# Performance work log

Hardware: AMD Instinct MI355X
Metric: run time of the kernel (lower is better)

The kernel has to match this reference:

```python
import jax, jax.numpy as jnp
import numpy as np

# Static problem dims (match setup_inputs / torch max()+1 derivation)
N = 2_000_000      # atoms
NALT = 8           # alternatives
B, C, R = 8, 4, 512  # batch, chains, residues
N_ATOM_TYPES = 500
VDW_COL = 0        # property_hashings['solvenergy_props']['VdW']
PADDING_INDEX = -1
BACKBONE_ATOMS = (0, 1, 2, 3)


def setup_inputs() -> dict:
    key = jax.random.key(0)
    k1, k2, k3, k4, k5, k6, k7, k8 = jax.random.split(key, 8)
    at_name = jax.random.randint(k1, (N,), 0, 40)      # atom type hashes (first 4 = backbone)
    batch = jax.random.randint(k2, (N,), 0, B)
    chain = jax.random.randint(k3, (N,), 0, C)
    resnum = jax.random.randint(k4, (N,), 0, R)
    atom_description = jnp.stack([at_name, batch, chain, resnum], axis=1).astype(jnp.int64)
    return {
        "coords": jax.random.normal(k5, (N, 3), dtype=jnp.float32),
        "atom_description": atom_description,
        "alternativeMask": jax.random.randint(k6, (N, NALT), 0, 2).astype(bool),
        "facc": jax.random.uniform(k7, (N, NALT), dtype=jnp.float32),
        "atom_Properties": jax.random.uniform(k8, (N_ATOM_TYPES, 8), dtype=jnp.float32),
        "weight": jnp.zeros((1,), dtype=jnp.float32),
    }


def reference(coords, atom_description, alternativeMask, facc, atom_Properties, weight):
    at_name = atom_description[:, 0]
    b_idx = atom_description[:, 1]
    c_idx = atom_description[:, 2]
    r_idx = atom_description[:, 3]

    # is_backbone: OR over backbone atom hashes
    bb = jnp.asarray(BACKBONE_ATOMS)
    is_backbone = (at_name[:, None] == bb[None, :]).any(axis=-1)  # [N]

    # bindToAtoms: gather VdW property, masked multiply by max(facc, 0)
    sa = jnp.maximum(facc, jnp.float32(0.0))                 # [N, NALT]
    vdw = atom_Properties[at_name, VDW_COL]                  # [N]
    atomE = jnp.where(alternativeMask, vdw[:, None] * sa, jnp.float32(0.0))
    atomE = atomE * (1.0 - jnp.tanh(weight[0])) * 0.3        # [N, NALT]

    # bindToResi: masked scatter-add into [B, C, R, NALT]
    valid = r_idx != PADDING_INDEX
    mc_vals = jnp.where((is_backbone & valid)[:, None], atomE, jnp.float32(0.0))
    sc_vals = jnp.where((~is_backbone & valid)[:, None], atomE, jnp.float32(0.0))
    zeros = jnp.zeros((B, C, R, NALT), dtype=jnp.float32)
    finalMC = zeros.at[b_idx, c_idx, r_idx].add(mc_vals)
    finalSC = zeros.at[b_idx, c_idx, r_idx].add(sc_vals)
    return finalMC, finalSC
```

## Files before the change

### kernel.cpp

```cpp
#include <hip/hip_runtime.h>
#include <hip/hip_bf16.h>
#include <math.h>

#define NALT      8
#define BDIM      8
#define CDIM      4
#define RDIM      512
#define OUT_HALF  (BDIM * CDIM * RDIM * NALT)
#define OUT_TOTAL (2 * OUT_HALF)

#define NBUCKET   32
#define BLK_ATOMS 1024
#define AITER     4
#define NWAVE     4
#define LSLOTS    8192


__device__ __forceinline__ unsigned int pack_bf16_2(float a, float b) {
    unsigned int ua = __float_as_uint(a);
    unsigned int ub = __float_as_uint(b);
    ua = (ua + 0x7fffu + ((ua >> 16) & 1u)) >> 16;
    ub = (ub + 0x7fffu + ((ub >> 16) & 1u)) >> 16;
    return ua | (ub << 16);
}

__global__ void __launch_bounds__(256) vdw_count_kernel(
    const int4*   __restrict__ desc,
    unsigned int* __restrict__ PW,
    unsigned short* __restrict__ hdr,
    int n)
{
    __shared__ unsigned int cw[NWAVE][NBUCKET];
    __shared__ unsigned int base[NBUCKET + 1];
    const int tid = threadIdx.x;
    const int w   = tid >> 6;
    if (tid < NWAVE * NBUCKET) cw[tid >> 5][tid & 31] = 0;
    __syncthreads();

    const int a0 = blockIdx.x * BLK_ATOMS;
    #pragma unroll
    for (int it = 0; it < AITER; ++it) {
        const int a = a0 + it * 256 + tid;
        if (a < n) {
            const int4 d = desc[a];
            if (d.w != -1) atomicAdd(&cw[w][d.y * CDIM + d.z], 1);
        }
    }
    __syncthreads();

    if (tid < NBUCKET) {
        unsigned int s = 0;
        unsigned int pref[NWAVE];
        #pragma unroll
        for (int ww = 0; ww < NWAVE; ++ww) { pref[ww] = s; s += cw[ww][tid]; }
        base[tid] = s;
        #pragma unroll
        for (int ww = 0; ww < NWAVE; ++ww) cw[ww][tid] = pref[ww];
    }
    __syncthreads();
    if (tid == 0) {
        unsigned int run = 0;
        #pragma unroll
        for (int j = 0; j < NBUCKET; ++j) { const unsigned int t = base[j]; base[j] = run; run += t; }
        base[NBUCKET] = run;
    }
    __syncthreads();

    if (tid < NBUCKET) {
        #pragma unroll
        for (int ww = 0; ww < NWAVE; ++ww)
            PW[(size_t)blockIdx.x * (NWAVE * NBUCKET) + ww * NBUCKET + tid] =
                base[tid] + cw[ww][tid];
    }
    if (tid <= NBUCKET) hdr[blockIdx.x * 64 + tid] = (unsigned short)base[tid];
}

__global__ void __launch_bounds__(256) vdw_compact_kernel(
    const int4*   __restrict__ desc,
    const int4*   __restrict__ mask,
    const float4* __restrict__ facc,
    const float*  __restrict__ props,
    const float*  __restrict__ weight,
    const unsigned int* __restrict__ PW,
    unsigned short* __restrict__ lidxArr,
    uint4*        __restrict__ valArr,
    int n)
{
    __shared__ unsigned short s_lidx[BLK_ATOMS];
    __shared__ uint4          s_val[BLK_ATOMS];
    __shared__ unsigned int   cw[NWAVE][NBUCKET];

    const int tid  = threadIdx.x;
    const int w    = tid >> 6;
    const int lane = tid & 63;
    if (lane < NBUCKET) cw[w][lane] = 0;

    const float scale = (1.0f - tanhf(weight[0])) * 0.3f;
    const int a0 = blockIdx.x * BLK_ATOMS;
    const unsigned int* myPW = PW + (size_t)blockIdx.x * (NWAVE * NBUCKET) + w * NBUCKET;

    int4   d_[AITER];
    float4 f0_[AITER], f1_[AITER];
    int4   m0_[AITER], m1_[AITER];
    bool   ok[AITER];
    #pragma unroll
    for (int it = 0; it < AITER; ++it) {
        const int a  = a0 + it * 256 + tid;
        ok[it] = (a < n);
        const int aa = ok[it] ? a : (n - 1);
        d_[it]  = desc[aa];
        f0_[it] = facc[aa * 2 + 0];
        f1_[it] = facc[aa * 2 + 1];
        m0_[it] = mask[aa * 2 + 0];
        m1_[it] = mask[aa * 2 + 1];
    }

    #pragma unroll
    for (int it = 0; it < AITER; ++it) {
        const int4 d = d_[it];
        if (!ok[it] || d.w == -1) continue;
        const int bkt  = d.y * CDIM + d.z;
        const float vs = props[d.x * 8] * scale;
        const int lidx = ((d.x < 4) ? 0 : 4096) + d.w * 8;

        const float4 f0 = f0_[it], f1 = f1_[it];
        const int4   m0 = m0_[it], m1 = m1_[it];
        const float v0 = m0.x ? vs * fmaxf(f0.x, 0.0f) : 0.0f;
        const float v1 = m0.y ? vs * fmaxf(f0.y, 0.0f) : 0.0f;
        const float v2 = m0.z ? vs * fmaxf(f0.z, 0.0f) : 0.0f;
        const float v3 = m0.w ? vs * fmaxf(f0.w, 0.0f) : 0.0f;
        const float v4 = m1.x ? vs * fmaxf(f1.x, 0.0f) : 0.0f;
        const float v5 = m1.y ? vs * fmaxf(f1.y, 0.0f) : 0.0f;
        const float v6 = m1.z ? vs * fmaxf(f1.z, 0.0f) : 0.0f;
        const float v7 = m1.w ? vs * fmaxf(f1.w, 0.0f) : 0.0f;

        const unsigned int rank = atomicAdd(&cw[w][bkt], 1u);
        const unsigned int pos  = myPW[bkt] + rank;
        s_lidx[pos] = (unsigned short)lidx;
        s_val[pos]  = make_uint4(pack_bf16_2(v0, v1), pack_bf16_2(v2, v3),
                                 pack_bf16_2(v4, v5), pack_bf16_2(v6, v7));
    }
    __syncthreads();

    unsigned int* ldst = (unsigned int*)(lidxArr + (size_t)blockIdx.x * BLK_ATOMS);
    const unsigned int* lsrc = (const unsigned int*)s_lidx;
    #pragma unroll
    for (int k = 0; k < BLK_ATOMS / 2 / 256; ++k)
        ldst[k * 256 + tid] = lsrc[k * 256 + tid];

    uint4* vdst = valArr + (size_t)blockIdx.x * BLK_ATOMS;
    #pragma unroll
    for (int k = 0; k < BLK_ATOMS / 256; ++k)
        vdst[k * 256 + tid] = s_val[k * 256 + tid];
}

__global__ void __launch_bounds__(256) vdw_accum_kernel(
    const unsigned short* __restrict__ hdrArr,
    const unsigned short* __restrict__ lidxArr,
    const uint4*          __restrict__ valArr,
    float*                __restrict__ partial,
    int nblocks, int nsplit)
{
    __shared__ float acc[LSLOTS];
    const int tid = threadIdx.x;
    for (int k = tid; k < LSLOTS; k += 256) acc[k] = 0.0f;
    __syncthreads();

    const int bucket = blockIdx.x / nsplit;
    const int split  = blockIdx.x % nsplit;
    const int per = (nblocks + nsplit - 1) / nsplit;
    const int b0  = split * per;
    const int b1  = (b0 + per < nblocks) ? (b0 + per) : nblocks;

    const int g    = tid >> 5;
    const int lane = tid & 31;

    for (int blk = b0 + g; blk < b1; blk += 8) {
        const int start = hdrArr[blk * 64 + bucket];
        const int end   = hdrArr[blk * 64 + bucket + 1];
        const unsigned short* la = lidxArr + (size_t)blk * BLK_ATOMS;
        const uint4*          va = valArr  + (size_t)blk * BLK_ATOMS;
        for (int rec = start + lane; rec < end; rec += 32) {
            const int   l = la[rec];
            const uint4 v = va[rec];
            float t;
            t = __uint_as_float(v.x << 16);          if (t != 0.0f) atomicAdd(&acc[l + 0], t);
            t = __uint_as_float(v.x & 0xffff0000u);  if (t != 0.0f) atomicAdd(&acc[l + 1], t);
            t = __uint_as_float(v.y << 16);          if (t != 0.0f) atomicAdd(&acc[l + 2], t);
            t = __uint_as_float(v.y & 0xffff0000u);  if (t != 0.0f) atomicAdd(&acc[l + 3], t);
            t = __uint_as_float(v.z << 16);          if (t != 0.0f) atomicAdd(&acc[l + 4], t);
            t = __uint_as_float(v.z & 0xffff0000u);  if (t != 0.0f) atomicAdd(&acc[l + 5], t);
            t = __uint_as_float(v.w << 16);          if (t != 0.0f) atomicAdd(&acc[l + 6], t);
            t = __uint_as_float(v.w & 0xffff0000u);  if (t != 0.0f) atomicAdd(&acc[l + 7], t);
        }
    }
    __syncthreads();

    float* dst = partial + (size_t)blockIdx.x * LSLOTS;
    for (int k = tid; k < LSLOTS; k += 256) dst[k] = acc[k];
}

__global__ void __launch_bounds__(256) vdw_merge_kernel(
    const float* __restrict__ partial,
    float*       __restrict__ out,
    int nsplit)
{
    const int idx = blockIdx.x * 256 + threadIdx.x;
    if (idx >= OUT_TOTAL) return;
    const int bb     = idx >> 17;
    const int b      = (idx >> 14) & 7;
    const int c      = (idx >> 12) & 3;
    const int lidx   = bb * 4096 + (idx & 4095);
    const int bucket = b * CDIM + c;
    const float* p = partial + ((size_t)bucket * nsplit) * LSLOTS + lidx;
    float s = 0.0f;
    for (int sp = 0; sp < nsplit; ++sp)
        s += p[(size_t)sp * LSLOTS];
    out[idx] = s;
}

__global__ void __launch_bounds__(256) vdw_atomic_kernel(
    const int*   __restrict__ desc,
    const int*   __restrict__ mask,
    const float* __restrict__ facc,
    const float* __restrict__ props,
    const float* __restrict__ weight,
    float*       __restrict__ out,
    int n)
{
    const int i = blockIdx.x * blockDim.x + threadIdx.x;
    if (i >= n) return;
    const float scale = (1.0f - tanhf(weight[0])) * 0.3f;
    const int4 d = reinterpret_cast<const int4*>(desc)[i];
    if (d.w == -1) return;
    const float vs = props[d.x * 8 + 0] * scale;
    const int   bb = (d.x >= 0 && d.x <= 3) ? 0 : 1;
    float* base = out + bb * OUT_HALF + (((d.y * CDIM + d.z) * RDIM + d.w) * NALT);
    const float4 f0 = reinterpret_cast<const float4*>(facc)[i * 2 + 0];
    const float4 f1 = reinterpret_cast<const float4*>(facc)[i * 2 + 1];
    const int4   m0 = reinterpret_cast<const int4*>(mask)[i * 2 + 0];
    const int4   m1 = reinterpret_cast<const int4*>(mask)[i * 2 + 1];
    if (m0.x) atomicAdd(base + 0, vs * fmaxf(f0.x, 0.0f));
    if (m0.y) atomicAdd(base + 1, vs * fmaxf(f0.y, 0.0f));
    if (m0.z) atomicAdd(base + 2, vs * fmaxf(f0.z, 0.0f));
    if (m0.w) atomicAdd(base + 3, vs * fmaxf(f0.w, 0.0f));
    if (m1.x) atomicAdd(base + 4, vs * fmaxf(f1.x, 0.0f));
    if (m1.y) atomicAdd(base + 5, vs * fmaxf(f1.y, 0.0f));
    if (m1.z) atomicAdd(base + 6, vs * fmaxf(f1.z, 0.0f));
    if (m1.w) atomicAdd(base + 7, vs * fmaxf(f1.w, 0.0f));
}

extern "C" void kernel_launch(void* const* d_in, const int* in_sizes, int n_in,
                              void* d_out, int out_size, void* d_ws, size_t ws_size,
                              hipStream_t stream)
{
    const int*   desc   = (const int*)d_in[1];
    const int*   mask   = (const int*)d_in[2];
    const float* facc   = (const float*)d_in[3];
    const float* props  = (const float*)d_in[4];
    const float* weight = (const float*)d_in[5];
    float*       out    = (float*)d_out;

    const int n       = in_sizes[1] / 4;
    const int nblocks = (n + BLK_ATOMS - 1) / BLK_ATOMS;

    auto align256 = [](size_t x) { return (x + 255) & ~(size_t)255; };
    const size_t off_pw   = 0;
    const size_t off_hdr  = align256(off_pw   + (size_t)nblocks * NWAVE * NBUCKET * 4);
    const size_t off_lidx = align256(off_hdr  + (size_t)nblocks * 64 * 2);
    const size_t off_val  = align256(off_lidx + (size_t)nblocks * BLK_ATOMS * 2);
    const size_t off_part = align256(off_val  + (size_t)nblocks * BLK_ATOMS * 16);

    int nsplit = 0;
    for (int cand = 16; cand >= 1; cand >>= 1) {
        const size_t need = off_part +
            (size_t)NBUCKET * cand * LSLOTS * sizeof(float);
        if (need <= ws_size) { nsplit = cand; break; }
    }

    if (nsplit >= 1) {
        char* ws = (char*)d_ws;
        unsigned int*   PWarr   = (unsigned int*)(ws + off_pw);
        unsigned short* hdrArr  = (unsigned short*)(ws + off_hdr);
        unsigned short* lidxArr = (unsigned short*)(ws + off_lidx);
        uint4*          valArr  = (uint4*)(ws + off_val);
        float*          part    = (float*)(ws + off_part);

        vdw_count_kernel<<<nblocks, 256, 0, stream>>>(
            (const int4*)desc, PWarr, hdrArr, n);

        vdw_compact_kernel<<<nblocks, 256, 0, stream>>>(
            (const int4*)desc, (const int4*)mask, (const float4*)facc,
            props, weight, PWarr, lidxArr, valArr, n);

        vdw_accum_kernel<<<NBUCKET * nsplit, 256, 0, stream>>>(
            hdrArr, lidxArr, valArr, part, nblocks, nsplit);

        vdw_merge_kernel<<<(OUT_TOTAL + 255) / 256, 256, 0, stream>>>(
            part, out, nsplit);
    } else {
        hipMemsetAsync(d_out, 0, (size_t)out_size * sizeof(float), stream);
        vdw_atomic_kernel<<<(n + 255) / 256, 256, 0, stream>>>(
            desc, mask, facc, props, weight, out, n);
    }
}
```

Measured before the change: 95.48 us.

## Fuse count into compact kernel and merge partials via last-block reduction

Result: slower. 180.9 us (+89.5%).

```diff
diff --git a/kernel.cpp b/kernel.cpp
--- a/kernel.cpp
+++ b/kernel.cpp
@@ -24,81 +24,29 @@
     return ua | (ub << 16);
 }
 
-__global__ void __launch_bounds__(256) vdw_count_kernel(
-    const int4*   __restrict__ desc,
-    unsigned int* __restrict__ PW,
-    unsigned short* __restrict__ hdr,
-    int n)
-{
-    __shared__ unsigned int cw[NWAVE][NBUCKET];
-    __shared__ unsigned int base[NBUCKET + 1];
-    const int tid = threadIdx.x;
-    const int w   = tid >> 6;
-    if (tid < NWAVE * NBUCKET) cw[tid >> 5][tid & 31] = 0;
-    __syncthreads();
-
-    const int a0 = blockIdx.x * BLK_ATOMS;
-    #pragma unroll
-    for (int it = 0; it < AITER; ++it) {
-        const int a = a0 + it * 256 + tid;
-        if (a < n) {
-            const int4 d = desc[a];
-            if (d.w != -1) atomicAdd(&cw[w][d.y * CDIM + d.z], 1);
-        }
-    }
-    __syncthreads();
-
-    if (tid < NBUCKET) {
-        unsigned int s = 0;
-        unsigned int pref[NWAVE];
-        #pragma unroll
-        for (int ww = 0; ww < NWAVE; ++ww) { pref[ww] = s; s += cw[ww][tid]; }
-        base[tid] = s;
-        #pragma unroll
-        for (int ww = 0; ww < NWAVE; ++ww) cw[ww][tid] = pref[ww];
-    }
-    __syncthreads();
-    if (tid == 0) {
-        unsigned int run = 0;
-        #pragma unroll
-        for (int j = 0; j < NBUCKET; ++j) { const unsigned int t = base[j]; base[j] = run; run += t; }
-        base[NBUCKET] = run;
-    }
-    __syncthreads();
-
-    if (tid < NBUCKET) {
-        #pragma unroll
-        for (int ww = 0; ww < NWAVE; ++ww)
-            PW[(size_t)blockIdx.x * (NWAVE * NBUCKET) + ww * NBUCKET + tid] =
-                base[tid] + cw[ww][tid];
-    }
-    if (tid <= NBUCKET) hdr[blockIdx.x * 64 + tid] = (unsigned short)base[tid];
-}
-
-__global__ void __launch_bounds__(256) vdw_compact_kernel(
+__global__ void __launch_bounds__(256) vdw_fused_kernel(
     const int4*   __restrict__ desc,
     const int4*   __restrict__ mask,
     const float4* __restrict__ facc,
     const float*  __restrict__ props,
     const float*  __restrict__ weight,
-    const unsigned int* __restrict__ PW,
+    unsigned short* __restrict__ hdrArr,
     unsigned short* __restrict__ lidxArr,
     uint4*        __restrict__ valArr,
     int n)
 {
+    __shared__ unsigned int   cw[NWAVE][NBUCKET];
+    __shared__ unsigned int   tot[NBUCKET];
+    __shared__ unsigned int   base[NBUCKET + 1];
     __shared__ unsigned short s_lidx[BLK_ATOMS];
     __shared__ uint4          s_val[BLK_ATOMS];
-    __shared__ unsigned int   cw[NWAVE][NBUCKET];
 
     const int tid  = threadIdx.x;
     const int w    = tid >> 6;
     const int lane = tid & 63;
     if (lane < NBUCKET) cw[w][lane] = 0;
 
-    const float scale = (1.0f - tanhf(weight[0])) * 0.3f;
     const int a0 = blockIdx.x * BLK_ATOMS;
-    const unsigned int* myPW = PW + (size_t)blockIdx.x * (NWAVE * NBUCKET) + w * NBUCKET;
-
     int4   d_[AITER];
     float4 f0_[AITER], f1_[AITER];
     int4   m0_[AITER], m1_[AITER];
@@ -114,15 +62,26 @@
         m0_[it] = mask[aa * 2 + 0];
         m1_[it] = mask[aa * 2 + 1];
     }
-
+    const float scale = (1.0f - tanhf(weight[0])) * 0.3f;
+
+    int bkt[AITER];
+    int lidx[AITER];
     #pragma unroll
     for (int it = 0; it < AITER; ++it) {
         const int4 d = d_[it];
-        if (!ok[it] || d.w == -1) continue;
-        const int bkt  = d.y * CDIM + d.z;
-        const float vs = props[d.x * 8] * scale;
-        const int lidx = ((d.x < 4) ? 0 : 4096) + d.w * 8;
-
+        bkt[it] = -1;
+        if (ok[it] && d.w != -1) {
+            bkt[it]  = d.y * CDIM + d.z;
+            lidx[it] = ((d.x < 4) ? 0 : 4096) + d.w * 8;
+            atomicAdd(&cw[w][bkt[it]], 1u);
+        }
+    }
+
+    uint4 rv[AITER];
+    #pragma unroll
+    for (int it = 0; it < AITER; ++it) {
+        if (bkt[it] < 0) continue;
+        const float vs = props[d_[it].x * 8] * scale;
         const float4 f0 = f0_[it], f1 = f1_[it];
         const int4   m0 = m0_[it], m1 = m1_[it];
         const float v0 = m0.x ? vs * fmaxf(f0.x, 0.0f) : 0.0f;
@@ -133,14 +92,41 @@
         const float v5 = m1.y ? vs * fmaxf(f1.y, 0.0f) : 0.0f;
         const float v6 = m1.z ? vs * fmaxf(f1.z, 0.0f) : 0.0f;
         const float v7 = m1.w ? vs * fmaxf(f1.w, 0.0f) : 0.0f;
-
-        const unsigned int rank = atomicAdd(&cw[w][bkt], 1u);
-        const unsigned int pos  = myPW[bkt] + rank;
-        s_lidx[pos] = (unsigned short)lidx;
-        s_val[pos]  = make_uint4(pack_bf16_2(v0, v1), pack_bf16_2(v2, v3),
-                                 pack_bf16_2(v4, v5), pack_bf16_2(v6, v7));
-    }
-    __syncthreads();
+        rv[it] = make_uint4(pack_bf16_2(v0, v1), pack_bf16_2(v2, v3),
+                            pack_bf16_2(v4, v5), pack_bf16_2(v6, v7));
+    }
+    __syncthreads();
+
+    if (tid < NBUCKET) {
+        unsigned int s = 0;
+        #pragma unroll
+        for (int ww = 0; ww < NWAVE; ++ww) {
+            const unsigned int c = cw[ww][tid];
+            cw[ww][tid] = s;
+            s += c;
+        }
+        tot[tid] = s;
+    }
+    __syncthreads();
+    if (tid == 0) {
+        unsigned int run = 0;
+        #pragma unroll
+        for (int j = 0; j < NBUCKET; ++j) { base[j] = run; run += tot[j]; }
+        base[NBUCKET] = run;
+    }
+    __syncthreads();
+
+    #pragma unroll
+    for (int it = 0; it < AITER; ++it) {
+        if (bkt[it] < 0) continue;
+        const unsigned int pos = base[bkt[it]] + atomicAdd(&cw[w][bkt[it]], 1u);
+        s_lidx[pos] = (unsigned short)lidx[it];
+        s_val[pos]  = rv[it];
+    }
+    __syncthreads();
+
+    if (tid <= NBUCKET)
+        hdrArr[blockIdx.x * 64 + tid] = (unsigned short)base[tid];
 
     unsigned int* ldst = (unsigned int*)(lidxArr + (size_t)blockIdx.x * BLK_ATOMS);
     const unsigned int* lsrc = (const unsigned int*)s_lidx;
@@ -154,14 +140,17 @@
         vdst[k * 256 + tid] = s_val[k * 256 + tid];
 }
 
-__global__ void __launch_bounds__(256) vdw_accum_kernel(
+__global__ void __launch_bounds__(256) vdw_accum_merge_kernel(
     const unsigned short* __restrict__ hdrArr,
     const unsigned short* __restrict__ lidxArr,
     const uint4*          __restrict__ valArr,
     float*                __restrict__ partial,
+    unsigned int*         __restrict__ done,
+    float*                __restrict__ out,
     int nblocks, int nsplit)
 {
     __shared__ float acc[LSLOTS];
+    __shared__ int   s_last;
     const int tid = threadIdx.x;
     for (int k = tid; k < LSLOTS; k += 256) acc[k] = 0.0f;
     __syncthreads();
@@ -198,25 +187,26 @@
 
     float* dst = partial + (size_t)blockIdx.x * LSLOTS;
     for (int k = tid; k < LSLOTS; k += 256) dst[k] = acc[k];
-}
-
-__global__ void __launch_bounds__(256) vdw_merge_kernel(
-    const float* __restrict__ partial,
-    float*       __restrict__ out,
-    int nsplit)
-{
-    const int idx = blockIdx.x * 256 + threadIdx.x;
-    if (idx >= OUT_TOTAL) return;
-    const int bb     = idx >> 17;
-    const int b      = (idx >> 14) & 7;
-    const int c      = (idx >> 12) & 3;
-    const int lidx   = bb * 4096 + (idx & 4095);
-    const int bucket = b * CDIM + c;
-    const float* p = partial + ((size_t)bucket * nsplit) * LSLOTS + lidx;
-    float s = 0.0f;
-    for (int sp = 0; sp < nsplit; ++sp)
-        s += p[(size_t)sp * LSLOTS];
-    out[idx] = s;
+    __threadfence();
+    if (tid == 0)
+        s_last = (atomicAdd(&done[bucket], 1u) == (unsigned int)(nsplit - 1));
+    __syncthreads();
+
+    if (s_last) {
+        __threadfence();
+        const int b = bucket >> 2;
+        const int c = bucket & 3;
+        for (int k = tid; k < LSLOTS; k += 256) {
+            float s = acc[k];
+            for (int sp = 0; sp < nsplit; ++sp) {
+                if (sp == split) continue;
+                s += partial[(size_t)(bucket * nsplit + sp) * LSLOTS + k];
+            }
+            const int bb    = k >> 12;
+            const int inner = k & 4095;
+            out[bb * OUT_HALF + b * (CDIM * RDIM * NALT) + c * 4096 + inner] = s;
+        }
+    }
 }
 
 __global__ void __launch_bounds__(256) vdw_atomic_kernel(
@@ -265,39 +255,37 @@
     const int nblocks = (n + BLK_ATOMS - 1) / BLK_ATOMS;
 
     auto align256 = [](size_t x) { return (x + 255) & ~(size_t)255; };
-    const size_t off_pw   = 0;
-    const size_t off_hdr  = align256(off_pw   + (size_t)nblocks * NWAVE * NBUCKET * 4);
+    const size_t off_hdr  = 0;
     const size_t off_lidx = align256(off_hdr  + (size_t)nblocks * 64 * 2);
     const size_t off_val  = align256(off_lidx + (size_t)nblocks * BLK_ATOMS * 2);
     const size_t off_part = align256(off_val  + (size_t)nblocks * BLK_ATOMS * 16);
 
     int nsplit = 0;
-    for (int cand = 16; cand >= 1; cand >>= 1) {
-        const size_t need = off_part +
-            (size_t)NBUCKET * cand * LSLOTS * sizeof(float);
-        if (need <= ws_size) { nsplit = cand; break; }
+    size_t off_done = 0;
+    for (int cand = 8; cand >= 1; cand >>= 1) {
+        const size_t pd = align256(off_part +
+            (size_t)NBUCKET * cand * LSLOTS * sizeof(float));
+        if (pd + NBUCKET * sizeof(unsigned int) <= ws_size) {
+            nsplit = cand; off_done = pd; break;
+        }
     }
 
     if (nsplit >= 1) {
         char* ws = (char*)d_ws;
-        unsigned int*   PWarr   = (unsigned int*)(ws + off_pw);
         unsigned short* hdrArr  = (unsigned short*)(ws + off_hdr);
         unsigned short* lidxArr = (unsigned short*)(ws + off_lidx);
         uint4*          valArr  = (uint4*)(ws + off_val);
         float*          part    = (float*)(ws + off_part);
-
-        vdw_count_kernel<<<nblocks, 256, 0, stream>>>(
-            (const int4*)desc, PWarr, hdrArr, n);
-
-        vdw_compact_kernel<<<nblocks, 256, 0, stream>>>(
+        unsigned int*   done    = (unsigned int*)(ws + off_done);
+
+        hipMemsetAsync(done, 0, NBUCKET * sizeof(unsigned int), stream);
+
+        vdw_fused_kernel<<<nblocks, 256, 0, stream>>>(
             (const int4*)desc, (const int4*)mask, (const float4*)facc,
-            props, weight, PWarr, lidxArr, valArr, n);
-
-        vdw_accum_kernel<<<NBUCKET * nsplit, 256, 0, stream>>>(
-            hdrArr, lidxArr, valArr, part, nblocks, nsplit);
-
-        vdw_merge_kernel<<<(OUT_TOTAL + 255) / 256, 256, 0, stream>>>(
-            part, out, nsplit);
+            props, weight, hdrArr, lidxArr, valArr, n);
+
+        vdw_accum_merge_kernel<<<NBUCKET * nsplit, 256, 0, stream>>>(
+            hdrArr, lidxArr, valArr, part, done, out, nblocks, nsplit);
     } else {
         hipMemsetAsync(d_out, 0, (size_t)out_size * sizeof(float), stream);
         vdw_atomic_kernel<<<(n + 255) / 256, 256, 0, stream>>>(
```
